# Performance work log

Measured on AMD Instinct MI355X. Metric: run time of the kernel, lower is better.

The kernel has to match this reference:

```python
import jax, jax.numpy as jnp
import numpy as np
import math

# D4 group multiplication permutations (rows of the 8x8 regular representation)
PERMS = (
    (0, 1, 2, 3, 4, 5, 6, 7),
    (3, 0, 1, 2, 5, 6, 7, 4),
    (2, 3, 0, 1, 6, 7, 4, 5),
    (1, 2, 3, 0, 7, 4, 5, 6),
    (4, 5, 6, 7, 0, 1, 2, 3),
    (5, 6, 7, 4, 3, 0, 1, 2),
    (6, 7, 4, 5, 2, 3, 0, 1),
    (7, 4, 5, 6, 1, 2, 3, 0),
)


def d4_1x1(x, w):
    """D4-equivariant 1x1 conv. x: (b, cin*8, h, w), w: (cout, cin, 8)."""
    b, C, h, ww = x.shape
    cout, cin, _ = w.shape
    # (cout, 8, cin, 8): permuted copies of the base weight
    W = jnp.stack([w[..., jnp.array(p)] for p in PERMS], axis=1)
    xr = x.reshape(b, cin, 8, h, ww)
    y = jnp.einsum('ogif,bifhw->boghw', W, xr)
    return y.reshape(b, cout * 8, h, ww)


def group_norm(x, gamma, beta, num_groups, eps=1e-5):
    b, C, h, w = x.shape
    xg = x.reshape(b, num_groups, C // num_groups, h, w)
    mean = xg.mean(axis=(2, 3, 4), keepdims=True)
    var = xg.var(axis=(2, 3, 4), keepdims=True)
    xn = ((xg - mean) / jnp.sqrt(var + eps)).reshape(b, C, h, w)
    return xn * gamma[None, :, None, None] + beta[None, :, None, None]


def unfold_patches(x, k):
    """torch.nn.Unfold(k, 1, (k-1)//2, 1) -> (b, C, k*k, h, w), patch idx = ki*k+kj."""
    b, C, h, w = x.shape
    p = (k - 1) // 2
    xp = jnp.pad(x, ((0, 0), (0, 0), (p, p), (p, p)))
    pats = jnp.stack([xp[:, :, i:i + h, j:j + w]
                      for i in range(k) for j in range(k)], axis=2)
    return pats


def setup_inputs() -> dict:
    key = jax.random.key(0)
    ks = jax.random.split(key, 4)
    b, H, W = 8, 56, 56
    cin, cout, rr, k, gc = 64, 64, 2, 3, 16
    cmid = cin // rr            # 32
    G = cout // gc              # 4 dynamic-kernel groups
    x = jax.random.normal(ks[0], (b, cin * 8, H, W), jnp.float32)
    w_v = jax.random.normal(ks[1], (cout, cin, 8), jnp.float32) / math.sqrt(8 * cin / 2)
    w1 = jax.random.normal(ks[2], (cmid, cin, 8), jnp.float32) / math.sqrt(8 * cin / 2)
    gn_gamma = jnp.ones((cmid * 8,), jnp.float32)
    gn_beta = jnp.zeros((cmid * 8,), jnp.float32)
    w2 = jax.random.normal(ks[3], (k * k * G, cmid), jnp.float32) / math.sqrt(cmid)
    b2 = jnp.zeros((k * k * G,), jnp.float32)
    return {"x": x, "w_v": w_v, "w1": w1, "gn_gamma": gn_gamma,
            "gn_beta": gn_beta, "w2": w2, "b2": b2}


def reference(x, w_v, w1, gn_gamma, gn_beta, w2, b2):
    k, gc = 3, 16
    b, _, h, w = x.shape
    cmid = w1.shape[0]
    G = w2.shape[0] // (k * k)
    # --- dynamic kernel branch: conv1 (D4 1x1 + GN + ReLU), conv2 (1x1x1 conv3d)
    t = jax.nn.relu(group_norm(d4_1x1(x, w1), gn_gamma, gn_beta, cmid))
    tr = t.reshape(b, cmid, 8, h, w)
    wgt = jnp.einsum('oi,bighw->boghw', w2, tr) + b2[None, :, None, None, None]
    wv = wgt.reshape(b, G, k, k, 8, h, w)
    # --- D4 symmetrization of the k x k kernel per group element
    s = [wv[:, :, :, :, g] for g in range(8)]          # each (b,G,k,k,h,w)
    sw = [jnp.swapaxes(s[g], 2, 3) for g in range(4, 8)]
    trans = [s[0],
             jnp.rot90(s[1], 1, (2, 3)),
             jnp.rot90(s[2], 2, (2, 3)),
             jnp.rot90(s[3], 3, (2, 3)),
             jnp.rot90(sw[0], 3, (2, 3)),
             jnp.rot90(sw[1], 2, (2, 3)),
             jnp.rot90(sw[2], 1, (2, 3)),
             sw[3]]
    wv = jnp.stack(trans, axis=4)                      # (b,G,k,k,8,h,w)
    wv = wv.reshape(b, G, k * k, 8, h, w)[:, :, None]  # (b,G,1,k^2,8,h,w)
    wv = jnp.swapaxes(wv, 3, 4)                        # (b,G,1,8,k^2,h,w)
    # --- value branch + unfold + multiply-sum
    xv = d4_1x1(x, w_v)                                # (b, cout*8, h, w)
    pats = unfold_patches(xv, k).reshape(b, G, gc, 8, k * k, h, w)
    out = (wv * pats).sum(axis=4)                      # (b,G,gc,8,h,w)
    return out.reshape(b, G * gc * 8, h, w)
```

## Files before the change

kernel.cpp:

```cpp
#include <hip/hip_runtime.h>

#define BATCH 8
#define PIX   3136
#define CIN8  512
#define CMID8 256
#define KDIM  512

typedef short short8 __attribute__((ext_vector_type(8)));
typedef float f32x4 __attribute__((ext_vector_type(4)));

__constant__ int c_perms[8][8] = {
    {0, 1, 2, 3, 4, 5, 6, 7},
    {3, 0, 1, 2, 5, 6, 7, 4},
    {2, 3, 0, 1, 6, 7, 4, 5},
    {1, 2, 3, 0, 7, 4, 5, 6},
    {4, 5, 6, 7, 0, 1, 2, 3},
    {5, 6, 7, 4, 3, 0, 1, 2},
    {6, 7, 4, 5, 2, 3, 0, 1},
};
__constant__ int c_perm7[8] = {7, 4, 5, 6, 1, 2, 3, 0};

__constant__ int c_tab[8][9] = {
    {0, 1, 2, 3, 4, 5, 6, 7, 8},
    {2, 5, 8, 1, 4, 7, 0, 3, 6},
    {8, 7, 6, 5, 4, 3, 2, 1, 0},
    {6, 3, 0, 7, 4, 1, 8, 5, 2},
    {2, 1, 0, 5, 4, 3, 8, 7, 6},
    {8, 5, 2, 7, 4, 1, 6, 3, 0},
    {6, 7, 8, 3, 4, 5, 0, 1, 2},
    {0, 3, 6, 1, 4, 7, 2, 5, 8},
};

__device__ __forceinline__ float bf2f(unsigned short u) {
    union { unsigned int i; float f; } v;
    v.i = ((unsigned int)u) << 16;
    return v.f;
}
__device__ __forceinline__ unsigned short f2bf(float f) {
    union { float f; unsigned int u; } v;
    v.f = f;
    unsigned int u = v.u;
    u += 0x7FFFu + ((u >> 16) & 1u);
    return (unsigned short)(u >> 16);
}
__device__ __forceinline__ float bflo(unsigned int u) {
    union { unsigned int i; float f; } v; v.i = u << 16; return v.f;
}
__device__ __forceinline__ float bfhi(unsigned int u) {
    union { unsigned int i; float f; } v; v.i = u & 0xFFFF0000u; return v.f;
}

__device__ __forceinline__ void gload_lds16(const unsigned short* g, unsigned short* l) {
    __builtin_amdgcn_global_load_lds(
        (const __attribute__((address_space(1))) unsigned int*)g,
        (__attribute__((address_space(3))) unsigned int*)l,
        16, 0, 0);
}

#define LDT 70
__global__ __launch_bounds__(256) void cvt_t_kernel(
    const float* __restrict__ x, unsigned short* __restrict__ xbfT)
{
    __shared__ unsigned short T[64 * LDT];
    const int flat = blockIdx.x;
    const int kt = flat & 7;
    const int pt = (flat >> 3) % 49;
    const int b  = flat / (49 * 8);
    const int k0 = kt * 64, p0 = pt * 64;

    const float* xb = x + ((size_t)b * CIN8 + k0) * PIX + p0;
    const int kl = threadIdx.x >> 4;
    const int pl = (threadIdx.x & 15) * 4;
#pragma unroll
    for (int pass = 0; pass < 4; ++pass) {
        int kk = kl + pass * 16;
        float4 v = *(const float4*)(xb + (size_t)kk * PIX + pl);
        ushort2 lo = {f2bf(v.x), f2bf(v.y)};
        ushort2 hi = {f2bf(v.z), f2bf(v.w)};
        *(ushort2*)&T[kk * LDT + pl]     = lo;
        *(ushort2*)&T[kk * LDT + pl + 2] = hi;
    }
    __syncthreads();
    const int prow = threadIdx.x >> 2;
    const int kc8  = (threadIdx.x & 3) * 8;
    unsigned short* ob = xbfT + ((size_t)b * PIX + p0 + prow) * KDIM + k0;
#pragma unroll
    for (int pass = 0; pass < 2; ++pass) {
        int kk = kc8 + pass * 32;
        unsigned short tmp[8];
#pragma unroll
        for (int j = 0; j < 8; ++j) tmp[j] = T[(kk + j) * LDT + prow];
        *(uint4*)(ob + kk) = *(const uint4*)tmp;
    }
}

__global__ __launch_bounds__(256) void build_w_kernel(
    const float* __restrict__ w_v, const float* __restrict__ w1,
    unsigned short* __restrict__ Wbig, float* __restrict__ stats2)
{
    if (blockIdx.x < 2) stats2[blockIdx.x * 256 + threadIdx.x] = 0.f;

    int idx = blockIdx.x * 256 + threadIdx.x;
    int r = idx >> 9;
    int k = idx & 511;
    int i = k >> 3, f = k & 7;
    float v;
    if (r < 512) {
        int o = r >> 3, g = r & 7;
        int pf = (g < 7) ? c_perms[g][f] : c_perm7[f];
        v = w_v[(o * 64 + i) * 8 + pf];
    } else {
        int rr = r - 512;
        int o = rr >> 3, g = rr & 7;
        int pf = (g < 7) ? c_perms[g][f] : c_perm7[f];
        v = w1[(o * 64 + i) * 8 + pf];
    }
    Wbig[idx] = f2bf(v);
}

__global__ __launch_bounds__(256, 5) void gemm_kernel(
    const unsigned short* __restrict__ xT,
    const unsigned short* __restrict__ Wbig,
    unsigned short* __restrict__ xv,
    float* __restrict__ y1,
    float* __restrict__ stats2)
{
    __shared__ unsigned short Wt[2][128 * 32];
    __shared__ unsigned short Xt[2][128 * 32];

    const int swz = (blockIdx.x & 7) * 147 + (blockIdx.x >> 3);
    const int rt  = swz % 6;
    const int pt  = swz / 6;
    const int row0 = rt * 128;
    const int P0   = pt * 128;

    const int tid  = threadIdx.x;
    const int lane = tid & 63;
    const int wave = tid >> 6;
    const int wm   = wave & 1;
    const int wn   = wave >> 1;

    f32x4 acc[4][4];
#pragma unroll
    for (int i = 0; i < 4; ++i)
#pragma unroll
        for (int j = 0; j < 4; ++j) acc[i][j] = (f32x4){0.f, 0.f, 0.f, 0.f};

    const int lr  = lane >> 2;
    const int lc  = lane & 3;
    const int qc0 = lc ^ ((lr >> 1) & 3);
    const unsigned short* wsrc = Wbig + (size_t)(row0 + wave * 32 + lr) * KDIM + qc0 * 8;
    const unsigned short* xsrc = xT + (size_t)(P0 + wave * 32 + lr) * KDIM + qc0 * 8;
    const int wofs = wave * 1024;

    const int m16 = lane & 15;
    const int lq  = lane >> 4;
    const int ckq = (lq ^ ((m16 >> 1) & 3)) * 8;

#define STAGE(buf, kt) do {                                                     \
    _Pragma("unroll")                                                           \
    for (int i = 0; i < 2; ++i) {                                               \
        gload_lds16(wsrc + (size_t)i * 16 * KDIM + (kt) * 32, &Wt[buf][wofs + i * 512]); \
        gload_lds16(xsrc + (size_t)i * 16 * KDIM + (kt) * 32, &Xt[buf][wofs + i * 512]); \
    }                                                                           \
} while (0)

    STAGE(0, 0);
    STAGE(1, 1);
    asm volatile("s_waitcnt vmcnt(4)\n\ts_barrier" ::: "memory");

    int cur = 0;
#pragma unroll 2
    for (int kc = 0; kc < 16; ++kc) {
        short8 bfrag[4];
#pragma unroll
        for (int nt = 0; nt < 4; ++nt)
            bfrag[nt] = *(const short8*)&Xt[cur][(wn * 64 + nt * 16 + m16) * 32 + ckq];
#pragma unroll
        for (int mt = 0; mt < 4; ++mt) {
            short8 afrag = *(const short8*)&Wt[cur][(wm * 64 + mt * 16 + m16) * 32 + ckq];
#pragma unroll
            for (int nt = 0; nt < 4; ++nt)
                acc[mt][nt] = __builtin_amdgcn_mfma_f32_16x16x32_bf16(
                    afrag, bfrag[nt], acc[mt][nt], 0, 0, 0);
        }
        if (kc == 15) break;

        asm volatile("s_barrier" ::: "memory");
        if (kc < 14) {
            STAGE(cur, kc + 2);
            asm volatile("s_waitcnt vmcnt(4)\n\ts_barrier" ::: "memory");
        } else {
            asm volatile("s_waitcnt vmcnt(0)\n\ts_barrier" ::: "memory");
        }
        cur ^= 1;
    }
#undef STAGE

    const int colw = P0 + wn * 64;
    const int bb   = colw / PIX;
    const int pq   = colw - bb * PIX;
    const int qm   = lq * 4;

    if (row0 < 512) {
        unsigned short* dst0 = xv + ((size_t)bb * CIN8) * PIX + pq + m16;
#pragma unroll
        for (int nt = 0; nt < 4; ++nt) {
            unsigned short* dst = dst0 + nt * 16;
#pragma unroll
            for (int mt = 0; mt < 4; ++mt) {
                const int m = row0 + wm * 64 + mt * 16 + qm;
#pragma unroll
                for (int r = 0; r < 4; ++r)
                    dst[(size_t)(m + r) * PIX] = f2bf(acc[mt][nt][r]);
            }
        }
    } else {
        float* dst0 = y1 + ((size_t)bb * CMID8) * PIX + pq + m16;
#pragma unroll
        for (int nt = 0; nt < 4; ++nt) {
            float* dst = dst0 + nt * 16;
#pragma unroll
            for (int mt = 0; mt < 4; ++mt) {
                const int m = (row0 - 512) + wm * 64 + mt * 16 + qm;
#pragma unroll
                for (int r = 0; r < 4; ++r)
                    dst[(size_t)(m + r) * PIX] = acc[mt][nt][r];
            }
        }
        const int gbase = ((row0 - 512) + wm * 64) >> 3;
#pragma unroll
        for (int mt = 0; mt < 4; ++mt) {
            float s = 0.f, ss = 0.f;
#pragma unroll
            for (int nt = 0; nt < 4; ++nt)
#pragma unroll
                for (int r = 0; r < 4; ++r) {
                    float v = acc[mt][nt][r];
                    s += v; ss += v * v;
                }
#pragma unroll
            for (int off = 1; off <= 16; off <<= 1) {
                s  += __shfl_xor(s, off);
                ss += __shfl_xor(ss, off);
            }
            if ((lane & 31) == 0) {
                const int g = gbase + 2 * mt + (lane >> 5);
                atomicAdd(&stats2[(bb * 32 + g) * 2],     s);
                atomicAdd(&stats2[(bb * 32 + g) * 2 + 1], ss);
            }
        }
    }
}

__global__ __launch_bounds__(256) void final_fused_kernel(
    const float* __restrict__ y1, const float* __restrict__ stats2,
    const float* __restrict__ gamma, const float* __restrict__ beta,
    const float* __restrict__ w2, const float* __restrict__ b2,
    const unsigned short* __restrict__ xv,
    float* __restrict__ out)
{
    const int swz  = (blockIdx.x & 7) * 128 + (blockIdx.x >> 3);
    const int combo = swz >> 2;
    const int b    = combo >> 5;
    const int g    = (combo >> 2) & 7;
    const int gidx = combo & 3;

    __shared__ float w2s[9 * 32];
    __shared__ float b2s9[9];
    __shared__ float scs[32], shs[32];
    const int tid = threadIdx.x;
    for (int i = tid; i < 288; i += 256) {
        int tt = i >> 5, ic = i & 31;
        w2s[i] = w2[(gidx * 9 + c_tab[g][tt]) * 32 + ic];
    }
    if (tid < 9) b2s9[tid] = b2[gidx * 9 + c_tab[g][tid]];
    if (tid < 32) {
        float S  = stats2[(b * 32 + tid) * 2];
        float SS = stats2[(b * 32 + tid) * 2 + 1];
        float mean = S * (1.f / 25088.f);
        float var  = SS * (1.f / 25088.f) - mean * mean;
        float rstd = rsqrtf(var + 1e-5f);
        float sc = rstd * gamma[tid * 8 + g];
        scs[tid] = sc;
        shs[tid] = beta[tid * 8 + g] - mean * sc;
    }
    __syncthreads();

    const int pp = (swz & 3) * 256 + tid;
    if (pp >= 784) return;
    const int p0 = pp * 4;
    const int h  = p0 / 56;
    const int w0 = p0 % 56;

    float wt[4][9];
#pragma unroll
    for (int i = 0; i < 4; ++i)
#pragma unroll
        for (int tt = 0; tt < 9; ++tt) wt[i][tt] = b2s9[tt];

    const float* yb = y1 + ((size_t)b * CMID8 + g) * PIX + p0;
#pragma unroll 4
    for (int ic = 0; ic < 32; ++ic) {
        float4 v = *(const float4*)(yb + (size_t)(ic * 8) * PIX);
        float t0 = v.x * scs[ic] + shs[ic]; t0 = t0 > 0.f ? t0 : 0.f;
        float t1 = v.y * scs[ic] + shs[ic]; t1 = t1 > 0.f ? t1 : 0.f;
        float t2 = v.z * scs[ic] + shs[ic]; t2 = t2 > 0.f ? t2 : 0.f;
        float t3 = v.w * scs[ic] + shs[ic]; t3 = t3 > 0.f ? t3 : 0.f;
#pragma unroll
        for (int tt = 0; tt < 9; ++tt) {
            float wv = w2s[tt * 32 + ic];
            wt[0][tt] = fmaf(wv, t0, wt[0][tt]);
            wt[1][tt] = fmaf(wv, t1, wt[1][tt]);
            wt[2][tt] = fmaf(wv, t2, wt[2][tt]);
            wt[3][tt] = fmaf(wv, t3, wt[3][tt]);
        }
    }

    int rb[3];
#pragma unroll
    for (int ki = 0; ki < 3; ++ki) {
        int hh = h + ki - 1;
        bool rv = (hh >= 0) & (hh < 56);
        int hc = hh < 0 ? 0 : (hh > 55 ? 55 : hh);
        rb[ki] = hc * 56;
        if (!rv) {
#pragma unroll
            for (int i = 0; i < 4; ++i)
#pragma unroll
                for (int kj = 0; kj < 3; ++kj) wt[i][ki * 3 + kj] = 0.f;
        }
    }
#pragma unroll
    for (int i = 0; i < 4; ++i)
#pragma unroll
        for (int tt = 0; tt < 9; ++tt) {
            int ww = w0 + i + (tt % 3) - 1;
            if (ww < 0 || ww >= 56) wt[i][tt] = 0.f;
        }

    const int c0 = (w0 == 0) ? 0 : (w0 - 2);

    const unsigned short* xc = xv + ((size_t)b * CIN8 + gidx * 128 + g) * PIX;
    float* ob = out + ((size_t)b * CIN8 + gidx * 128 + g) * PIX + p0;
#pragma unroll 2
    for (int cc = 0; cc < 16; ++cc) {
        f32x4 a = (f32x4){0.f, 0.f, 0.f, 0.f};
#pragma unroll
        for (int ki = 0; ki < 3; ++ki) {
            const unsigned short* row = xc + rb[ki];
            unsigned int u0 = *(const unsigned int*)(row + c0);
            unsigned int u1 = *(const unsigned int*)(row + w0);
            unsigned int u2 = *(const unsigned int*)(row + w0 + 2);
            unsigned int u3 = *(const unsigned int*)(row + w0 + 4);
            float f1 = bfhi(u0);
            float f2 = bflo(u1), f3 = bfhi(u1);
            float f4 = bflo(u2), f5 = bfhi(u2);
            float f6 = bflo(u3);
            const int t0i = ki * 3;
            a[0] = fmaf(wt[0][t0i + 0], f1, a[0]);
            a[0] = fmaf(wt[0][t0i + 1], f2, a[0]);
            a[0] = fmaf(wt[0][t0i + 2], f3, a[0]);
            a[1] = fmaf(wt[1][t0i + 0], f2, a[1]);
            a[1] = fmaf(wt[1][t0i + 1], f3, a[1]);
            a[1] = fmaf(wt[1][t0i + 2], f4, a[1]);
            a[2] = fmaf(wt[2][t0i + 0], f3, a[2]);
            a[2] = fmaf(wt[2][t0i + 1], f4, a[2]);
            a[2] = fmaf(wt[2][t0i + 2], f5, a[2]);
            a[3] = fmaf(wt[3][t0i + 0], f4, a[3]);
            a[3] = fmaf(wt[3][t0i + 1], f5, a[3]);
            a[3] = fmaf(wt[3][t0i + 2], f6, a[3]);
        }
        *(f32x4*)(ob + (size_t)cc * 8 * PIX) = a;
        xc += (size_t)8 * PIX;
    }
}

extern "C" void kernel_launch(void* const* d_in, const int* in_sizes, int n_in,
                              void* d_out, int out_size, void* d_ws, size_t ws_size,
                              hipStream_t stream) {
    (void)in_sizes; (void)n_in; (void)out_size; (void)ws_size;
    const float* x     = (const float*)d_in[0];
    const float* w_v   = (const float*)d_in[1];
    const float* w1    = (const float*)d_in[2];
    const float* gamma = (const float*)d_in[3];
    const float* beta  = (const float*)d_in[4];
    const float* w2    = (const float*)d_in[5];
    const float* b2    = (const float*)d_in[6];
    float* out = (float*)d_out;

    char* ws = (char*)d_ws;
    unsigned short* Wbig = (unsigned short*)ws;
    unsigned short* xbfT = (unsigned short*)(ws + 786432);
    unsigned short* xv   = (unsigned short*)(ws + 26476544);
    float* y1     = (float*)(ws + 52166656);
    float* stats2 = (float*)(ws + 77856768);

    cvt_t_kernel<<<3136, 256, 0, stream>>>(x, xbfT);
    build_w_kernel<<<1536, 256, 0, stream>>>(w_v, w1, Wbig, stats2);
    gemm_kernel<<<1176, 256, 0, stream>>>(xbfT, Wbig, xv, y1, stats2);
    final_fused_kernel<<<256 * 4, 256, 0, stream>>>(
        y1, stats2, gamma, beta, w2, b2, xv, out);
}
```

Baseline: 187.8 us.

## Store y1 in bf16, merge prep kernels, relax gemm occupancy and barriers

The intermediate y1 activation is now written and read as bf16 instead of fp32, halving its traffic between the GEMM and the final fused kernel. The weight-build kernel is merged into the transpose/convert kernel as extra blocks, removing one launch. The GEMM launch-bounds occupancy hint drops from 5 to 4, the unroll-2 pragma is removed, and inline-asm barriers become builtins. Storing y1 in bf16 adds rounding error to the group-norm input, although the statistics are still accumulated from fp32 values.

```diff
diff --git a/kernel.cpp b/kernel.cpp
--- a/kernel.cpp
+++ b/kernel.cpp
@@ -58,10 +58,35 @@
 }
 
 #define LDT 70
-__global__ __launch_bounds__(256) void cvt_t_kernel(
-    const float* __restrict__ x, unsigned short* __restrict__ xbfT)
+__global__ __launch_bounds__(256) void prep_kernel(
+    const float* __restrict__ x, unsigned short* __restrict__ xbfT,
+    const float* __restrict__ w_v, const float* __restrict__ w1,
+    unsigned short* __restrict__ Wbig, float* __restrict__ stats2)
 {
     __shared__ unsigned short T[64 * LDT];
+
+    if (blockIdx.x >= 3136) {
+        const int bid = blockIdx.x - 3136;
+        if (bid < 2) stats2[bid * 256 + threadIdx.x] = 0.f;
+        int idx = bid * 256 + threadIdx.x;
+        int r = idx >> 9;
+        int k = idx & 511;
+        int i = k >> 3, f = k & 7;
+        float v;
+        if (r < 512) {
+            int o = r >> 3, g = r & 7;
+            int pf = (g < 7) ? c_perms[g][f] : c_perm7[f];
+            v = w_v[(o * 64 + i) * 8 + pf];
+        } else {
+            int rr = r - 512;
+            int o = rr >> 3, g = rr & 7;
+            int pf = (g < 7) ? c_perms[g][f] : c_perm7[f];
+            v = w1[(o * 64 + i) * 8 + pf];
+        }
+        Wbig[idx] = f2bf(v);
+        return;
+    }
+
     const int flat = blockIdx.x;
     const int kt = flat & 7;
     const int pt = (flat >> 3) % 49;
@@ -94,35 +119,11 @@
     }
 }
 
-__global__ __launch_bounds__(256) void build_w_kernel(
-    const float* __restrict__ w_v, const float* __restrict__ w1,
-    unsigned short* __restrict__ Wbig, float* __restrict__ stats2)
-{
-    if (blockIdx.x < 2) stats2[blockIdx.x * 256 + threadIdx.x] = 0.f;
-
-    int idx = blockIdx.x * 256 + threadIdx.x;
-    int r = idx >> 9;
-    int k = idx & 511;
-    int i = k >> 3, f = k & 7;
-    float v;
-    if (r < 512) {
-        int o = r >> 3, g = r & 7;
-        int pf = (g < 7) ? c_perms[g][f] : c_perm7[f];
-        v = w_v[(o * 64 + i) * 8 + pf];
-    } else {
-        int rr = r - 512;
-        int o = rr >> 3, g = rr & 7;
-        int pf = (g < 7) ? c_perms[g][f] : c_perm7[f];
-        v = w1[(o * 64 + i) * 8 + pf];
-    }
-    Wbig[idx] = f2bf(v);
-}
-
-__global__ __launch_bounds__(256, 5) void gemm_kernel(
+__global__ __launch_bounds__(256, 4) void gemm_kernel(
     const unsigned short* __restrict__ xT,
     const unsigned short* __restrict__ Wbig,
     unsigned short* __restrict__ xv,
-    float* __restrict__ y1,
+    unsigned short* __restrict__ y1b,
     float* __restrict__ stats2)
 {
     __shared__ unsigned short Wt[2][128 * 32];
@@ -167,10 +168,10 @@
 
     STAGE(0, 0);
     STAGE(1, 1);
-    asm volatile("s_waitcnt vmcnt(4)\n\ts_barrier" ::: "memory");
+    asm volatile("s_waitcnt vmcnt(4)" ::: "memory");
+    __builtin_amdgcn_s_barrier();
 
     int cur = 0;
-#pragma unroll 2
     for (int kc = 0; kc < 16; ++kc) {
         short8 bfrag[4];
 #pragma unroll
@@ -186,13 +187,14 @@
         }
         if (kc == 15) break;
 
-        asm volatile("s_barrier" ::: "memory");
+        __builtin_amdgcn_s_barrier();
         if (kc < 14) {
             STAGE(cur, kc + 2);
-            asm volatile("s_waitcnt vmcnt(4)\n\ts_barrier" ::: "memory");
+            asm volatile("s_waitcnt vmcnt(4)" ::: "memory");
         } else {
-            asm volatile("s_waitcnt vmcnt(0)\n\ts_barrier" ::: "memory");
-        }
+            asm volatile("s_waitcnt vmcnt(0)" ::: "memory");
+        }
+        __builtin_amdgcn_s_barrier();
         cur ^= 1;
     }
 #undef STAGE
@@ -216,16 +218,16 @@
             }
         }
     } else {
-        float* dst0 = y1 + ((size_t)bb * CMID8) * PIX + pq + m16;
+        unsigned short* dst0 = y1b + ((size_t)bb * CMID8) * PIX + pq + m16;
 #pragma unroll
         for (int nt = 0; nt < 4; ++nt) {
-            float* dst = dst0 + nt * 16;
+            unsigned short* dst = dst0 + nt * 16;
 #pragma unroll
             for (int mt = 0; mt < 4; ++mt) {
                 const int m = (row0 - 512) + wm * 64 + mt * 16 + qm;
 #pragma unroll
                 for (int r = 0; r < 4; ++r)
-                    dst[(size_t)(m + r) * PIX] = acc[mt][nt][r];
+                    dst[(size_t)(m + r) * PIX] = f2bf(acc[mt][nt][r]);
             }
         }
         const int gbase = ((row0 - 512) + wm * 64) >> 3;
@@ -254,7 +256,7 @@
 }
 
 __global__ __launch_bounds__(256) void final_fused_kernel(
-    const float* __restrict__ y1, const float* __restrict__ stats2,
+    const unsigned short* __restrict__ y1b, const float* __restrict__ stats2,
     const float* __restrict__ gamma, const float* __restrict__ beta,
     const float* __restrict__ w2, const float* __restrict__ b2,
     const unsigned short* __restrict__ xv,
@@ -299,14 +301,14 @@
 #pragma unroll
         for (int tt = 0; tt < 9; ++tt) wt[i][tt] = b2s9[tt];
 
-    const float* yb = y1 + ((size_t)b * CMID8 + g) * PIX + p0;
+    const unsigned short* yb = y1b + ((size_t)b * CMID8 + g) * PIX + p0;
 #pragma unroll 4
     for (int ic = 0; ic < 32; ++ic) {
-        float4 v = *(const float4*)(yb + (size_t)(ic * 8) * PIX);
-        float t0 = v.x * scs[ic] + shs[ic]; t0 = t0 > 0.f ? t0 : 0.f;
-        float t1 = v.y * scs[ic] + shs[ic]; t1 = t1 > 0.f ? t1 : 0.f;
-        float t2 = v.z * scs[ic] + shs[ic]; t2 = t2 > 0.f ? t2 : 0.f;
-        float t3 = v.w * scs[ic] + shs[ic]; t3 = t3 > 0.f ? t3 : 0.f;
+        uint2 u = *(const uint2*)(yb + (size_t)(ic * 8) * PIX);
+        float t0 = bflo(u.x) * scs[ic] + shs[ic]; t0 = t0 > 0.f ? t0 : 0.f;
+        float t1 = bfhi(u.x) * scs[ic] + shs[ic]; t1 = t1 > 0.f ? t1 : 0.f;
+        float t2 = bflo(u.y) * scs[ic] + shs[ic]; t2 = t2 > 0.f ? t2 : 0.f;
+        float t3 = bfhi(u.y) * scs[ic] + shs[ic]; t3 = t3 > 0.f ? t3 : 0.f;
 #pragma unroll
         for (int tt = 0; tt < 9; ++tt) {
             float wv = w2s[tt * 32 + ic];
@@ -393,12 +395,11 @@
     unsigned short* Wbig = (unsigned short*)ws;
     unsigned short* xbfT = (unsigned short*)(ws + 786432);
     unsigned short* xv   = (unsigned short*)(ws + 26476544);
-    float* y1     = (float*)(ws + 52166656);
-    float* stats2 = (float*)(ws + 77856768);
-
-    cvt_t_kernel<<<3136, 256, 0, stream>>>(x, xbfT);
-    build_w_kernel<<<1536, 256, 0, stream>>>(w_v, w1, Wbig, stats2);
-    gemm_kernel<<<1176, 256, 0, stream>>>(xbfT, Wbig, xv, y1, stats2);
+    unsigned short* y1b  = (unsigned short*)(ws + 52166656);
+    float* stats2 = (float*)(ws + 65011712);
+
+    prep_kernel<<<3136 + 1536, 256, 0, stream>>>(x, xbfT, w_v, w1, Wbig, stats2);
+    gemm_kernel<<<1176, 256, 0, stream>>>(xbfT, Wbig, xv, y1b, stats2);
     final_fused_kernel<<<256 * 4, 256, 0, stream>>>(
-        y1, stats2, gamma, beta, w2, b2, xv, out);
-}
+        y1b, stats2, gamma, beta, w2, b2, xv, out);
+}
```

Result: faster. 164.0 us, median of 2 (-12.7%).
